# Optimization experiments

Measured on AMD Instinct MI355X. Metric: run time of the kernel, lower is better.

Reference implementation:

```python
import jax, jax.numpy as jnp
import numpy as np

NEG_INF = -1e30

def setup_inputs() -> dict:
    key = jax.random.key(0)
    k1, k2, k3, k4, k5 = jax.random.split(key, 5)
    B, N, Fin, Fout, H = 8, 1024, 128, 64, 4
    h = jax.random.normal(k1, (B, N, Fin), dtype=jnp.float32)
    adj = jax.random.randint(k2, (N, N), 0, 2, dtype=jnp.int32)
    bias_matrix = jax.random.normal(k3, (1, 1, N, N), dtype=jnp.float32)
    # xavier-ish scaled params
    W = jax.random.normal(k4, (H, Fin, Fout), dtype=jnp.float32) * (1.0 / np.sqrt(Fin))
    a = jax.random.normal(k5, (H, 2 * Fout, 1), dtype=jnp.float32) * (1.0 / np.sqrt(2 * Fout))
    return {"h": h, "adj": adj, "bias_matrix": bias_matrix, "W": W, "a": a}


def reference(h, adj, bias_matrix, W, a):
    B, N, _ = h.shape
    H, _, Fout = W.shape
    # h_prime: [B, N, H, Fout]
    h_prime = jnp.einsum('bni,hio->bnho', h, W)
    # split attention vector: a_input @ a == h_i @ a1 + h_j @ a2 (same math, no O(N^2*F) tensor)
    a1 = a[:, :Fout, 0]   # [H, Fout]
    a2 = a[:, Fout:, 0]   # [H, Fout]
    ei = jnp.einsum('bnhf,hf->bnh', h_prime, a1)  # [B, N, H]
    ej = jnp.einsum('bnhf,hf->bnh', h_prime, a2)  # [B, N, H]
    e = jax.nn.leaky_relu(ei[:, :, None, :] + ej[:, None, :, :], negative_slope=0.2)  # [B,N,N,H]
    # bias_matrix [1,1,N,N] -> expand to [B,1,N,N] -> permute(0,2,3,1) -> [B,N,N,1]
    bias = jnp.transpose(bias_matrix, (0, 2, 3, 1))  # [1, N, N, 1], broadcasts to [B,N,N,H]
    e = e + bias
    mask = (adj != 0)[None, :, :, None]  # [1, N, N, 1]
    e_masked = jnp.where(mask, e, NEG_INF)
    attention = jax.nn.softmax(e_masked, axis=2)  # softmax over j
    h_out = jnp.einsum('bijh,bjhf->bihf', attention, h_prime)  # [B, N, H, Fout]
    return h_out.reshape(B, N, H * Fout)
```

## Files before the change

### kernel.cpp

```cpp
#include <hip/hip_runtime.h>

constexpr int B = 8, N = 1024, FIN = 128, FOUT = 64, H = 4;
constexpr float LOG2E = 1.44269504f;

typedef __attribute__((ext_vector_type(8))) short short8;
typedef __attribute__((ext_vector_type(4))) short short4v;
typedef __attribute__((ext_vector_type(4))) float f32x4;

static __device__ inline unsigned short f2bf(float x) {
    union { float f; unsigned u; } v; v.f = x;
    unsigned r = v.u + 0x7fff + ((v.u >> 16) & 1);
    return (unsigned short)(r >> 16);
}

__global__ __launch_bounds__(256) void gat_prep(
    const float* __restrict__ h,
    const float* __restrict__ W,
    const float* __restrict__ a,
    const int*   __restrict__ adj,
    const float* __restrict__ bias,
    unsigned short* __restrict__ hpF,
    unsigned short* __restrict__ mbB,
    float* __restrict__ ei_t,
    float* __restrict__ ej_t)
{
    __shared__ float h_lds[32][132];
    const int t = threadIdx.x;

    if (blockIdx.x < 512) {
        unsigned short* mlds = reinterpret_cast<unsigned short*>(h_lds);
        const int bx = blockIdx.x;
        const int ti = bx >> 3;
        const int j0 = (bx & 7) * 128;

        const int r = t >> 4;
        const int g = t & 15;
        const size_t src = (size_t)(ti * 16 + r) * N + j0 + g * 8;
        const int4*   ap = reinterpret_cast<const int4*>(adj + src);
        const float4* bp = reinterpret_cast<const float4*>(bias + src);
        int4   a0 = ap[0], a1 = ap[1];
        float4 b0 = bp[0], b1 = bp[1];
        unsigned short q0 = f2bf(a0.x ? LOG2E * b0.x : -1e35f);
        unsigned short q1 = f2bf(a0.y ? LOG2E * b0.y : -1e35f);
        unsigned short q2 = f2bf(a0.z ? LOG2E * b0.z : -1e35f);
        unsigned short q3 = f2bf(a0.w ? LOG2E * b0.w : -1e35f);
        unsigned short q4 = f2bf(a1.x ? LOG2E * b1.x : -1e35f);
        unsigned short q5 = f2bf(a1.y ? LOG2E * b1.y : -1e35f);
        unsigned short q6 = f2bf(a1.z ? LOG2E * b1.z : -1e35f);
        unsigned short q7 = f2bf(a1.w ? LOG2E * b1.w : -1e35f);
        int4 ov;
        ov.x = (int)((unsigned)q0 | ((unsigned)q1 << 16));
        ov.y = (int)((unsigned)q2 | ((unsigned)q3 << 16));
        ov.z = (int)((unsigned)q4 | ((unsigned)q5 << 16));
        ov.w = (int)((unsigned)q6 | ((unsigned)q7 << 16));
        *reinterpret_cast<int4*>(&mlds[r * 128 + ((g ^ (r & 7)) * 8)]) = ov;
        __syncthreads();

        const int w    = t >> 6;
        const int lane = t & 63;
        const int li   = lane & 15;
        const int kg   = lane >> 4;
        const int gr   = w * 4 + kg;
        int4 ov2 = *reinterpret_cast<const int4*>(
            &mlds[li * 128 + ((gr ^ (li & 7)) * 8)]);
        const int jc = (bx & 7) * 4 + w;
        *reinterpret_cast<int4*>(mbB + (((size_t)ti * 32 + jc) * 64 + lane) * 8) = ov2;
        return;
    }

    const int blk = blockIdx.x - 512;
    const int b   = blk >> 5;
    const int n0  = (blk & 31) * 32;

    {
        const float* src = h + ((size_t)b * N + n0) * FIN;
        for (int v = t; v < 1024; v += 256) {
            float4 x = reinterpret_cast<const float4*>(src)[v];
            int fl = v * 4;
            *reinterpret_cast<float4*>(&h_lds[fl >> 7][fl & 127]) = x;
        }
    }

    const int hd   = t >> 6;
    const int lane = t & 63;
    const int li   = lane & 15;
    const int kg   = lane >> 4;

    short8 wf[4][4];
    {
        const float* Wp = W + (size_t)hd * FIN * FOUT;
        #pragma unroll
        for (int ks = 0; ks < 4; ++ks)
            #pragma unroll
            for (int ft = 0; ft < 4; ++ft) {
                const float* wb = Wp + (size_t)(ks * 32 + 8 * kg) * FOUT + 16 * ft + li;
                int4 pk_;
                float u0 = wb[0],       u1 = wb[64],      u2 = wb[128], u3 = wb[192];
                float u4 = wb[256],     u5 = wb[320],     u6 = wb[384], u7 = wb[448];
                asm("v_cvt_pk_bf16_f32 %0, %1, %2" : "=v"(pk_.x) : "v"(u0), "v"(u1));
                asm("v_cvt_pk_bf16_f32 %0, %1, %2" : "=v"(pk_.y) : "v"(u2), "v"(u3));
                asm("v_cvt_pk_bf16_f32 %0, %1, %2" : "=v"(pk_.z) : "v"(u4), "v"(u5));
                asm("v_cvt_pk_bf16_f32 %0, %1, %2" : "=v"(pk_.w) : "v"(u6), "v"(u7));
                wf[ks][ft] = *reinterpret_cast<short8*>(&pk_);
            }
    }
    __syncthreads();

    f32x4 c[4][2];
    #pragma unroll
    for (int ft = 0; ft < 4; ++ft)
        #pragma unroll
        for (int rt = 0; rt < 2; ++rt) c[ft][rt] = f32x4{0.f, 0.f, 0.f, 0.f};

    #pragma unroll
    for (int rt = 0; rt < 2; ++rt) {
        #pragma unroll
        for (int ks = 0; ks < 4; ++ks) {
            const float* hp8 = &h_lds[16 * rt + li][ks * 32 + 8 * kg];
            float4 x0 = *reinterpret_cast<const float4*>(hp8);
            float4 x1 = *reinterpret_cast<const float4*>(hp8 + 4);
            int4 pk_;
            asm("v_cvt_pk_bf16_f32 %0, %1, %2" : "=v"(pk_.x) : "v"(x0.x), "v"(x0.y));
            asm("v_cvt_pk_bf16_f32 %0, %1, %2" : "=v"(pk_.y) : "v"(x0.z), "v"(x0.w));
            asm("v_cvt_pk_bf16_f32 %0, %1, %2" : "=v"(pk_.z) : "v"(x1.x), "v"(x1.y));
            asm("v_cvt_pk_bf16_f32 %0, %1, %2" : "=v"(pk_.w) : "v"(x1.z), "v"(x1.w));
            short8 af = *reinterpret_cast<short8*>(&pk_);
            c[0][rt] = __builtin_amdgcn_mfma_f32_16x16x32_bf16(af, wf[ks][0], c[0][rt], 0, 0, 0);
            c[1][rt] = __builtin_amdgcn_mfma_f32_16x16x32_bf16(af, wf[ks][1], c[1][rt], 0, 0, 0);
            c[2][rt] = __builtin_amdgcn_mfma_f32_16x16x32_bf16(af, wf[ks][2], c[2][rt], 0, 0, 0);
            c[3][rt] = __builtin_amdgcn_mfma_f32_16x16x32_bf16(af, wf[ks][3], c[3][rt], 0, 0, 0);
        }
    }

    const int bh = b * H + hd;
    const int jc = n0 >> 5;
    #pragma unroll
    for (int ft = 0; ft < 4; ++ft)
        #pragma unroll
        for (int rt = 0; rt < 2; ++rt) {
            short4v v4;
            v4[0] = (short)f2bf(c[ft][rt][0]);
            v4[1] = (short)f2bf(c[ft][rt][1]);
            v4[2] = (short)f2bf(c[ft][rt][2]);
            v4[3] = (short)f2bf(c[ft][rt][3]);
            const int lanep = li + 16 * (2 * rt + (kg >> 1));
            *reinterpret_cast<short4v*>(
                hpF + ((((size_t)bh * 32 + jc) * 4 + ft) * 64 + lanep) * 8 + 4 * (kg & 1)) = v4;
        }

    float a1v[4], a2v[4];
    #pragma unroll
    for (int ft = 0; ft < 4; ++ft) {
        a1v[ft] = a[(size_t)hd * 2 * FOUT + 16 * ft + li];
        a2v[ft] = a[(size_t)hd * 2 * FOUT + FOUT + 16 * ft + li];
    }
    #pragma unroll
    for (int rt = 0; rt < 2; ++rt)
        #pragma unroll
        for (int r = 0; r < 4; ++r) {
            float e1 = c[0][rt][r] * a1v[0] + c[1][rt][r] * a1v[1]
                     + c[2][rt][r] * a1v[2] + c[3][rt][r] * a1v[3];
            float e2 = c[0][rt][r] * a2v[0] + c[1][rt][r] * a2v[1]
                     + c[2][rt][r] * a2v[2] + c[3][rt][r] * a2v[3];
            #pragma unroll
            for (int m = 1; m < 16; m <<= 1) {
                e1 += __shfl_xor(e1, m, 64);
                e2 += __shfl_xor(e2, m, 64);
            }
            if (li == 0) {
                int rr = n0 + 16 * rt + 4 * kg + r;
                ei_t[(size_t)bh * N + rr] = LOG2E * e1;
                ej_t[(size_t)bh * N + rr] = LOG2E * e2;
            }
        }
}

__global__ __launch_bounds__(512) void gat_attn(
    const unsigned short* __restrict__ hpF,
    const float* __restrict__ ei_t,
    const float* __restrict__ ej_t,
    const unsigned short* __restrict__ mbB,
    float* __restrict__ out)
{
    __shared__ __align__(16) char smem[32768];
    typedef unsigned short hstage_t[2][4][512];
    hstage_t* hstage = reinterpret_cast<hstage_t*>(smem);

    const int raw  = blockIdx.x;
    const int xcd  = raw & 7;
    const int k_   = raw >> 3;
    const int bh   = ((xcd >> 1) << 3) | (k_ >> 3);
    const int it0  = (((xcd & 1) << 3) | (k_ & 7)) * 4;
    const int t    = threadIdx.x;
    const int w8   = t >> 6;
    const int w    = w8 & 3;
    const int jh   = w8 >> 2;
    const int lane = t & 63;
    const int li   = lane & 15;
    const int kg   = lane >> 4;
    const int ti   = it0 + w;
    const int irow = ti * 16 + li;
    const int jcb  = jh * 16;

    const float  ei0   = ei_t[(size_t)bh * N + irow];
    const float* ejrow = ej_t + (size_t)bh * N;
    const unsigned short* mrow = mbB + ((size_t)ti * 32 * 64 + lane) * 8;
    const size_t hbase = (size_t)bh * 65536;

    f32x4 c0 = {0.f,0.f,0.f,0.f}, c1 = {0.f,0.f,0.f,0.f};
    f32x4 c2 = {0.f,0.f,0.f,0.f}, c3 = {0.f,0.f,0.f,0.f};
    f32x4 c4 = {0.f,0.f,0.f,0.f};
    const short obf = (short)0x3F80;
    const short8 ones = {obf,obf,obf,obf,obf,obf,obf,obf};

    #define VMCNT6() asm volatile("s_waitcnt vmcnt(6)" ::: "memory")
    #define BARRIER() { __builtin_amdgcn_s_barrier(); asm volatile("" ::: "memory"); }

    #define STAGE(BUF, JCG) {                                                 \
        const unsigned short* gs_ = hpF + hbase + (size_t)(JCG) * 2048        \
                                        + (size_t)w * 512 + (size_t)lane * 8; \
        __builtin_amdgcn_global_load_lds(                                     \
            (const __attribute__((address_space(1))) void*)gs_,               \
            (__attribute__((address_space(3))) void*)&hstage[BUF][jh][w][0],  \
            16, 0, 0); }

    #define REGS(S, JCG) {                                                    \
        mq##S  = *reinterpret_cast<const int4*>(mrow + (size_t)(JCG) * 512);  \
        ejA##S = *reinterpret_cast<const float4*>(ejrow + (JCG) * 32 + 8 * kg);\
        ejB##S = *reinterpret_cast<const float4*>(ejrow + (JCG) * 32 + 8 * kg + 4); }

    #define DSREAD(BUF, BA, BB, BC, BD) {                                     \
        BA = *reinterpret_cast<const short8*>(&hstage[BUF][jh][0][lane * 8]); \
        BB = *reinterpret_cast<const short8*>(&hstage[BUF][jh][1][lane * 8]); \
        BC = *reinterpret_cast<const short8*>(&hstage[BUF][jh][2][lane * 8]); \
        BD = *reinterpret_cast<const short8*>(&hstage[BUF][jh][3][lane * 8]); }

    #define SCORE2(PL, PH, EJL, EJH, QW) {                                    \
        float bl_ = __uint_as_float(((unsigned)(QW)) << 16);                  \
        float bh_ = __uint_as_float(((unsigned)(QW)) & 0xffff0000u);          \
        float el_ = ei0 + (EJL); el_ = fmaxf(el_, 0.2f * el_) + bl_;          \
        float eh_ = ei0 + (EJH); eh_ = fmaxf(eh_, 0.2f * eh_) + bh_;          \
        asm("v_exp_f32 %0, %1" : "=v"(PL) : "v"(el_));                        \
        asm("v_exp_f32 %0, %1" : "=v"(PH) : "v"(eh_)); }

    #define COMPS(S, BA, BB, BC, BD) {                                        \
        float p0,p1,p2,p3,p4,p5,p6,p7;                                        \
        SCORE2(p0, p1, ejA##S.x, ejA##S.y, mq##S.x)                           \
        SCORE2(p2, p3, ejA##S.z, ejA##S.w, mq##S.y)                           \
        SCORE2(p4, p5, ejB##S.x, ejB##S.y, mq##S.z)                           \
        SCORE2(p6, p7, ejB##S.z, ejB##S.w, mq##S.w)                           \
        int4 pk_;                                                             \
        asm("v_cvt_pk_bf16_f32 %0, %1, %2" : "=v"(pk_.x) : "v"(p0), "v"(p1)); \
        asm("v_cvt_pk_bf16_f32 %0, %1, %2" : "=v"(pk_.y) : "v"(p2), "v"(p3)); \
        asm("v_cvt_pk_bf16_f32 %0, %1, %2" : "=v"(pk_.z) : "v"(p4), "v"(p5)); \
        asm("v_cvt_pk_bf16_f32 %0, %1, %2" : "=v"(pk_.w) : "v"(p6), "v"(p7)); \
        short8 a0_ = *reinterpret_cast<short8*>(&pk_);                        \
        c0 = __builtin_amdgcn_mfma_f32_16x16x32_bf16(a0_, BA, c0, 0, 0, 0);   \
        c1 = __builtin_amdgcn_mfma_f32_16x16x32_bf16(a0_, BB, c1, 0, 0, 0);   \
        c2 = __builtin_amdgcn_mfma_f32_16x16x32_bf16(a0_, BC, c2, 0, 0, 0);   \
        c3 = __builtin_amdgcn_mfma_f32_16x16x32_bf16(a0_, BD, c3, 0, 0, 0);   \
        c4 = __builtin_amdgcn_mfma_f32_16x16x32_bf16(a0_, ones, c4, 0, 0, 0); }

    short8 A0, B0, C0, D0, A1, B1, C1, D1;
    int4 mq0, mq1;
    float4 ejA0, ejB0, ejA1, ejB1;

    STAGE(0, jcb + 0)
    STAGE(1, jcb + 1)
    REGS(0, jcb + 0)
    REGS(1, jcb + 1)
    VMCNT6();
    BARRIER();

    #pragma unroll 1
    for (int k = 0; k < 16; k += 2) {
        const int pa = (k + 2 < 16) ? jcb + k + 2 : jcb + 15;
        const int pb = (k + 3 < 16) ? jcb + k + 3 : jcb + 15;
        const int ba = k & 2 ? 2 : 0;
        const int bb = ba + 1;
        const int bn0 = ba ^ 2;
        const int bn1 = bb ^ 2;
        STAGE(bn0, pa)
        STAGE(bn1, pb)
        DSREAD(ba, A0, B0, C0, D0)
        COMPS(0, A0, B0, C0, D0)
        REGS(0, pa)
        DSREAD(bb, A1, B1, C1, D1)
        COMPS(1, A1, B1, C1, D1)
        REGS(1, pb)
        VMCNT6();
        BARRIER();
    }
    #undef VMCNT6
    #undef BARRIER
    #undef STAGE
    #undef REGS
    #undef DSREAD
    #undef SCORE2
    #undef COMPS

    f32x4 (*red)[4][64] = reinterpret_cast<f32x4 (*)[4][64]>(smem);

    __syncthreads();
    if (jh == 1) {
        red[0][w][lane] = c0;
        red[1][w][lane] = c1;
        red[2][w][lane] = c2;
        red[3][w][lane] = c3;
        red[4][w][lane] = c4;
    }
    __syncthreads();
    if (jh == 1) return;

    c0 += red[0][w][lane];
    c1 += red[1][w][lane];
    c2 += red[2][w][lane];
    c3 += red[3][w][lane];
    c4 += red[4][w][lane];

    const int b  = bh >> 2;
    const int hd = bh & 3;
    #pragma unroll
    for (int r = 0; r < 4; ++r) {
        int orow = ti * 16 + 4 * kg + r;
        float inv = 1.0f / c4[r];
        float* ob = out + (((size_t)b * N + orow) * H + hd) * 64 + li;
        ob[0]  = c0[r] * inv;
        ob[16] = c1[r] * inv;
        ob[32] = c2[r] * inv;
        ob[48] = c3[r] * inv;
    }
}

extern "C" void kernel_launch(void* const* d_in, const int* in_sizes, int n_in,
                              void* d_out, int out_size, void* d_ws, size_t ws_size,
                              hipStream_t stream) {
    const float* h    = (const float*)d_in[0];
    const int*   adj  = (const int*)  d_in[1];
    const float* bias = (const float*)d_in[2];
    const float* W    = (const float*)d_in[3];
    const float* a    = (const float*)d_in[4];
    float* out = (float*)d_out;

    char* ws = (char*)d_ws;
    unsigned short* hpF = (unsigned short*)ws;
    unsigned short* mbB = (unsigned short*)(ws + ((size_t)4 << 20));
    float* ei_t = (float*)(ws + ((size_t)6 << 20));
    float* ej_t = ei_t + (size_t)B * H * N;

    gat_prep<<<512 + B * N / 32, 256, 0, stream>>>(h, W, a, adj, bias,
                                                   hpF, mbB, ei_t, ej_t);
    gat_attn<<<B * H * (N / 64), 512, 0, stream>>>(hpF, ei_t, ej_t, mbB, out);
}
```

Measured before the change: 34.40 us.

## Split key dimension four ways with two row tiles per wave in attention kernel

Reorganises gat_attn so each of the 8 waves handles two 16-row query tiles over one quarter of the key range, instead of one row tile over half the key range. Each staged V fragment read from LDS now feeds two sets of MFMAs, which halves LDS reads per MFMA, and the loop runs 8 single-step iterations instead of 16 paired ones. The cost is a larger cross-wave reduction through 60 KB of shared memory (three partial sums per output), more accumulator registers per wave, and only two stage buffers of depth, which may reduce occupancy and prefetch slack.

Measured after the change: 34.09 us (median of 2 runs). No clear change (-0.9%).

```diff
diff --git a/kernel.cpp b/kernel.cpp
--- a/kernel.cpp
+++ b/kernel.cpp
@@ -182,8 +182,8 @@
     const unsigned short* __restrict__ mbB,
     float* __restrict__ out)
 {
-    __shared__ __align__(16) char smem[32768];
-    typedef unsigned short hstage_t[2][4][512];
+    __shared__ __align__(16) char smem[61440];
+    typedef unsigned short hstage_t[4][4][512];
     hstage_t* hstage = reinterpret_cast<hstage_t*>(smem);
 
     const int raw  = blockIdx.x;
@@ -193,142 +193,164 @@
     const int it0  = (((xcd & 1) << 3) | (k_ & 7)) * 4;
     const int t    = threadIdx.x;
     const int w8   = t >> 6;
-    const int w    = w8 & 3;
-    const int jh   = w8 >> 2;
+    const int isup = w8 & 1;
+    const int jq   = w8 >> 1;
     const int lane = t & 63;
     const int li   = lane & 15;
     const int kg   = lane >> 4;
-    const int ti   = it0 + w;
-    const int irow = ti * 16 + li;
-    const int jcb  = jh * 16;
-
-    const float  ei0   = ei_t[(size_t)bh * N + irow];
+    const int tiA  = it0 + 2 * isup;
+    const int tiB  = tiA + 1;
+    const int jqb  = jq * 8;
+
+    const float ei0a = ei_t[(size_t)bh * N + tiA * 16 + li];
+    const float ei0b = ei_t[(size_t)bh * N + tiB * 16 + li];
     const float* ejrow = ej_t + (size_t)bh * N;
-    const unsigned short* mrow = mbB + ((size_t)ti * 32 * 64 + lane) * 8;
+    const unsigned short* mrowA = mbB + ((size_t)tiA * 32 * 64 + lane) * 8;
+    const unsigned short* mrowB = mbB + ((size_t)tiB * 32 * 64 + lane) * 8;
     const size_t hbase = (size_t)bh * 65536;
 
-    f32x4 c0 = {0.f,0.f,0.f,0.f}, c1 = {0.f,0.f,0.f,0.f};
-    f32x4 c2 = {0.f,0.f,0.f,0.f}, c3 = {0.f,0.f,0.f,0.f};
-    f32x4 c4 = {0.f,0.f,0.f,0.f};
+    f32x4 cA0 = {0,0,0,0}, cA1 = {0,0,0,0}, cA2 = {0,0,0,0}, cA3 = {0,0,0,0};
+    f32x4 cB0 = {0,0,0,0}, cB1 = {0,0,0,0}, cB2 = {0,0,0,0}, cB3 = {0,0,0,0};
+    f32x4 c4a = {0,0,0,0}, c4b = {0,0,0,0};
     const short obf = (short)0x3F80;
     const short8 ones = {obf,obf,obf,obf,obf,obf,obf,obf};
 
-    #define VMCNT6() asm volatile("s_waitcnt vmcnt(6)" ::: "memory")
+    #define VMCNT4() asm volatile("s_waitcnt vmcnt(4)" ::: "memory")
     #define BARRIER() { __builtin_amdgcn_s_barrier(); asm volatile("" ::: "memory"); }
 
-    #define STAGE(BUF, JCG) {                                                 \
-        const unsigned short* gs_ = hpF + hbase + (size_t)(JCG) * 2048        \
-                                        + (size_t)w * 512 + (size_t)lane * 8; \
-        __builtin_amdgcn_global_load_lds(                                     \
-            (const __attribute__((address_space(1))) void*)gs_,               \
-            (__attribute__((address_space(3))) void*)&hstage[BUF][jh][w][0],  \
+    #define STAGE(BUF, JCG) {                                                   \
+        const unsigned short* g0_ = hpF + hbase + (size_t)(JCG) * 2048          \
+                                  + (size_t)(2 * isup) * 512 + (size_t)lane * 8;\
+        __builtin_amdgcn_global_load_lds(                                       \
+            (const __attribute__((address_space(1))) void*)g0_,                 \
+            (__attribute__((address_space(3))) void*)&hstage[BUF][jq][2 * isup][0], \
+            16, 0, 0);                                                          \
+        __builtin_amdgcn_global_load_lds(                                       \
+            (const __attribute__((address_space(1))) void*)(g0_ + 512),         \
+            (__attribute__((address_space(3))) void*)&hstage[BUF][jq][2 * isup + 1][0], \
             16, 0, 0); }
 
-    #define REGS(S, JCG) {                                                    \
-        mq##S  = *reinterpret_cast<const int4*>(mrow + (size_t)(JCG) * 512);  \
-        ejA##S = *reinterpret_cast<const float4*>(ejrow + (JCG) * 32 + 8 * kg);\
-        ejB##S = *reinterpret_cast<const float4*>(ejrow + (JCG) * 32 + 8 * kg + 4); }
-
-    #define DSREAD(BUF, BA, BB, BC, BD) {                                     \
-        BA = *reinterpret_cast<const short8*>(&hstage[BUF][jh][0][lane * 8]); \
-        BB = *reinterpret_cast<const short8*>(&hstage[BUF][jh][1][lane * 8]); \
-        BC = *reinterpret_cast<const short8*>(&hstage[BUF][jh][2][lane * 8]); \
-        BD = *reinterpret_cast<const short8*>(&hstage[BUF][jh][3][lane * 8]); }
-
-    #define SCORE2(PL, PH, EJL, EJH, QW) {                                    \
-        float bl_ = __uint_as_float(((unsigned)(QW)) << 16);                  \
-        float bh_ = __uint_as_float(((unsigned)(QW)) & 0xffff0000u);          \
-        float el_ = ei0 + (EJL); el_ = fmaxf(el_, 0.2f * el_) + bl_;          \
-        float eh_ = ei0 + (EJH); eh_ = fmaxf(eh_, 0.2f * eh_) + bh_;          \
-        asm("v_exp_f32 %0, %1" : "=v"(PL) : "v"(el_));                        \
+    #define REGS(JCG) {                                                         \
+        mqA  = *reinterpret_cast<const int4*>(mrowA + (size_t)(JCG) * 512);     \
+        mqB  = *reinterpret_cast<const int4*>(mrowB + (size_t)(JCG) * 512);     \
+        ejA  = *reinterpret_cast<const float4*>(ejrow + (JCG) * 32 + 8 * kg);   \
+        ejB  = *reinterpret_cast<const float4*>(ejrow + (JCG) * 32 + 8 * kg + 4); }
+
+    #define DSREAD(BUF) {                                                       \
+        V0 = *reinterpret_cast<const short8*>(&hstage[BUF][jq][0][lane * 8]);   \
+        V1 = *reinterpret_cast<const short8*>(&hstage[BUF][jq][1][lane * 8]);   \
+        V2 = *reinterpret_cast<const short8*>(&hstage[BUF][jq][2][lane * 8]);   \
+        V3 = *reinterpret_cast<const short8*>(&hstage[BUF][jq][3][lane * 8]); }
+
+    #define SCORE2(PL, PH, EI, EJL, EJH, QW) {                                  \
+        float bl_ = __uint_as_float(((unsigned)(QW)) << 16);                    \
+        float bh_ = __uint_as_float(((unsigned)(QW)) & 0xffff0000u);            \
+        float el_ = (EI) + (EJL); el_ = fmaxf(el_, 0.2f * el_) + bl_;           \
+        float eh_ = (EI) + (EJH); eh_ = fmaxf(eh_, 0.2f * eh_) + bh_;           \
+        asm("v_exp_f32 %0, %1" : "=v"(PL) : "v"(el_));                          \
         asm("v_exp_f32 %0, %1" : "=v"(PH) : "v"(eh_)); }
 
-    #define COMPS(S, BA, BB, BC, BD) {                                        \
-        float p0,p1,p2,p3,p4,p5,p6,p7;                                        \
-        SCORE2(p0, p1, ejA##S.x, ejA##S.y, mq##S.x)                           \
-        SCORE2(p2, p3, ejA##S.z, ejA##S.w, mq##S.y)                           \
-        SCORE2(p4, p5, ejB##S.x, ejB##S.y, mq##S.z)                           \
-        SCORE2(p6, p7, ejB##S.z, ejB##S.w, mq##S.w)                           \
-        int4 pk_;                                                             \
-        asm("v_cvt_pk_bf16_f32 %0, %1, %2" : "=v"(pk_.x) : "v"(p0), "v"(p1)); \
-        asm("v_cvt_pk_bf16_f32 %0, %1, %2" : "=v"(pk_.y) : "v"(p2), "v"(p3)); \
-        asm("v_cvt_pk_bf16_f32 %0, %1, %2" : "=v"(pk_.z) : "v"(p4), "v"(p5)); \
-        asm("v_cvt_pk_bf16_f32 %0, %1, %2" : "=v"(pk_.w) : "v"(p6), "v"(p7)); \
-        short8 a0_ = *reinterpret_cast<short8*>(&pk_);                        \
-        c0 = __builtin_amdgcn_mfma_f32_16x16x32_bf16(a0_, BA, c0, 0, 0, 0);   \
-        c1 = __builtin_amdgcn_mfma_f32_16x16x32_bf16(a0_, BB, c1, 0, 0, 0);   \
-        c2 = __builtin_amdgcn_mfma_f32_16x16x32_bf16(a0_, BC, c2, 0, 0, 0);   \
-        c3 = __builtin_amdgcn_mfma_f32_16x16x32_bf16(a0_, BD, c3, 0, 0, 0);   \
-        c4 = __builtin_amdgcn_mfma_f32_16x16x32_bf16(a0_, ones, c4, 0, 0, 0); }
-
-    short8 A0, B0, C0, D0, A1, B1, C1, D1;
-    int4 mq0, mq1;
-    float4 ejA0, ejB0, ejA1, ejB1;
-
-    STAGE(0, jcb + 0)
-    STAGE(1, jcb + 1)
-    REGS(0, jcb + 0)
-    REGS(1, jcb + 1)
-    VMCNT6();
+    #define AFRAG(DST, EI, MQ) {                                                \
+        float p0,p1,p2,p3,p4,p5,p6,p7;                                          \
+        SCORE2(p0, p1, EI, ejA.x, ejA.y, MQ.x)                                  \
+        SCORE2(p2, p3, EI, ejA.z, ejA.w, MQ.y)                                  \
+        SCORE2(p4, p5, EI, ejB.x, ejB.y, MQ.z)                                  \
+        SCORE2(p6, p7, EI, ejB.z, ejB.w, MQ.w)                                  \
+        int4 pk_;                                                               \
+        asm("v_cvt_pk_bf16_f32 %0, %1, %2" : "=v"(pk_.x) : "v"(p0), "v"(p1));   \
+        asm("v_cvt_pk_bf16_f32 %0, %1, %2" : "=v"(pk_.y) : "v"(p2), "v"(p3));   \
+        asm("v_cvt_pk_bf16_f32 %0, %1, %2" : "=v"(pk_.z) : "v"(p4), "v"(p5));   \
+        asm("v_cvt_pk_bf16_f32 %0, %1, %2" : "=v"(pk_.w) : "v"(p6), "v"(p7));   \
+        DST = *reinterpret_cast<short8*>(&pk_); }
+
+    #define COMPS() {                                                           \
+        short8 aA_, aB_;                                                        \
+        AFRAG(aA_, ei0a, mqA)                                                   \
+        cA0 = __builtin_amdgcn_mfma_f32_16x16x32_bf16(aA_, V0, cA0, 0, 0, 0);   \
+        cA1 = __builtin_amdgcn_mfma_f32_16x16x32_bf16(aA_, V1, cA1, 0, 0, 0);   \
+        cA2 = __builtin_amdgcn_mfma_f32_16x16x32_bf16(aA_, V2, cA2, 0, 0, 0);   \
+        cA3 = __builtin_amdgcn_mfma_f32_16x16x32_bf16(aA_, V3, cA3, 0, 0, 0);   \
+        c4a = __builtin_amdgcn_mfma_f32_16x16x32_bf16(aA_, ones, c4a, 0, 0, 0); \
+        AFRAG(aB_, ei0b, mqB)                                                   \
+        cB0 = __builtin_amdgcn_mfma_f32_16x16x32_bf16(aB_, V0, cB0, 0, 0, 0);   \
+        cB1 = __builtin_amdgcn_mfma_f32_16x16x32_bf16(aB_, V1, cB1, 0, 0, 0);   \
+        cB2 = __builtin_amdgcn_mfma_f32_16x16x32_bf16(aB_, V2, cB2, 0, 0, 0);   \
+        cB3 = __builtin_amdgcn_mfma_f32_16x16x32_bf16(aB_, V3, cB3, 0, 0, 0);   \
+        c4b = __builtin_amdgcn_mfma_f32_16x16x32_bf16(aB_, ones, c4b, 0, 0, 0); }
+
+    short8 V0, V1, V2, V3;
+    int4 mqA, mqB;
+    float4 ejA, ejB;
+
+    STAGE(0, jqb)
+    REGS(jqb)
+    VMCNT4();
     BARRIER();
 
     #pragma unroll 1
-    for (int k = 0; k < 16; k += 2) {
-        const int pa = (k + 2 < 16) ? jcb + k + 2 : jcb + 15;
-        const int pb = (k + 3 < 16) ? jcb + k + 3 : jcb + 15;
-        const int ba = k & 2 ? 2 : 0;
-        const int bb = ba + 1;
-        const int bn0 = ba ^ 2;
-        const int bn1 = bb ^ 2;
-        STAGE(bn0, pa)
-        STAGE(bn1, pb)
-        DSREAD(ba, A0, B0, C0, D0)
-        COMPS(0, A0, B0, C0, D0)
-        REGS(0, pa)
-        DSREAD(bb, A1, B1, C1, D1)
-        COMPS(1, A1, B1, C1, D1)
-        REGS(1, pb)
-        VMCNT6();
+    for (int k = 0; k < 8; ++k) {
+        const int nxt = (k + 1 < 8) ? jqb + k + 1 : jqb + 7;
+        STAGE((k + 1) & 1, nxt)
+        DSREAD(k & 1)
+        COMPS()
+        REGS(nxt)
+        VMCNT4();
         BARRIER();
     }
-    #undef VMCNT6
+    #undef VMCNT4
     #undef BARRIER
     #undef STAGE
     #undef REGS
     #undef DSREAD
     #undef SCORE2
+    #undef AFRAG
     #undef COMPS
 
-    f32x4 (*red)[4][64] = reinterpret_cast<f32x4 (*)[4][64]>(smem);
+    f32x4 (*red)[2][10][64] = reinterpret_cast<f32x4 (*)[2][10][64]>(smem);
 
     __syncthreads();
-    if (jh == 1) {
-        red[0][w][lane] = c0;
-        red[1][w][lane] = c1;
-        red[2][w][lane] = c2;
-        red[3][w][lane] = c3;
-        red[4][w][lane] = c4;
+    if (jq != 0) {
+        f32x4 (*slot)[64] = red[jq - 1][isup];
+        slot[0][lane] = cA0; slot[1][lane] = cA1;
+        slot[2][lane] = cA2; slot[3][lane] = cA3;
+        slot[4][lane] = cB0; slot[5][lane] = cB1;
+        slot[6][lane] = cB2; slot[7][lane] = cB3;
+        slot[8][lane] = c4a; slot[9][lane] = c4b;
     }
     __syncthreads();
-    if (jh == 1) return;
-
-    c0 += red[0][w][lane];
-    c1 += red[1][w][lane];
-    c2 += red[2][w][lane];
-    c3 += red[3][w][lane];
-    c4 += red[4][w][lane];
+    if (jq != 0) return;
+
+    #pragma unroll
+    for (int s = 0; s < 3; ++s) {
+        f32x4 (*slot)[64] = red[s][isup];
+        cA0 += slot[0][lane]; cA1 += slot[1][lane];
+        cA2 += slot[2][lane]; cA3 += slot[3][lane];
+        cB0 += slot[4][lane]; cB1 += slot[5][lane];
+        cB2 += slot[6][lane]; cB3 += slot[7][lane];
+        c4a += slot[8][lane]; c4b += slot[9][lane];
+    }
 
     const int b  = bh >> 2;
     const int hd = bh & 3;
     #pragma unroll
     for (int r = 0; r < 4; ++r) {
-        int orow = ti * 16 + 4 * kg + r;
-        float inv = 1.0f / c4[r];
+        int orow = tiA * 16 + 4 * kg + r;
+        float inv = 1.0f / c4a[r];
         float* ob = out + (((size_t)b * N + orow) * H + hd) * 64 + li;
-        ob[0]  = c0[r] * inv;
-        ob[16] = c1[r] * inv;
-        ob[32] = c2[r] * inv;
-        ob[48] = c3[r] * inv;
+        ob[0]  = cA0[r] * inv;
+        ob[16] = cA1[r] * inv;
+        ob[32] = cA2[r] * inv;
+        ob[48] = cA3[r] * inv;
+    }
+    #pragma unroll
+    for (int r = 0; r < 4; ++r) {
+        int orow = tiB * 16 + 4 * kg + r;
+        float inv = 1.0f / c4b[r];
+        float* ob = out + (((size_t)b * N + orow) * H + hd) * 64 + li;
+        ob[0]  = cB0[r] * inv;
+        ob[16] = cB1[r] * inv;
+        ob[32] = cB2[r] * inv;
+        ob[48] = cB3[r] * inv;
     }
 }
 
```
